# Kernel tuning notes

Hardware: AMD Instinct MI355X
Metric: run time of the kernel (lower is better)

Reference implementation:

```python
import jax, jax.numpy as jnp
import numpy as np

POS_THR = 0.01
EXPANSION = 0.3
HW_RATIO = 2.0


def setup_inputs() -> dict:
    key = jax.random.key(0)
    kp, kj, kv, kg, km = jax.random.split(key, 5)
    B, P, K, H, W = 16, 20, 17, 160, 160
    hm_pred = jax.random.uniform(kp, (B, K, H, W), dtype=jnp.float32)  # some above POS_THR
    gt = jax.random.uniform(kg, (B, K, H, W), dtype=jnp.float32)
    xy = jax.random.uniform(kj, (B, P, K, 2), dtype=jnp.float32) * jnp.array([W, H], jnp.float32)
    v = (jax.random.uniform(kv, (B, P, K, 1)) > 0.3).astype(jnp.float32)
    jointsXYV = jnp.concatenate([xy, v], axis=-1)
    masks = (jax.random.uniform(km, (B, H, W)) > 0.02).astype(jnp.float32)
    return {"hm_pred": hm_pred, "jointsXYV": jointsXYV, "masks": masks, "gt": gt}


def _gen_hm_mask(hm_pred, masks, jointsXYV):
    # hm_pred: [B,K,H,W]; masks: [B,H,W]; jointsXYV: [B,P,K,3]
    B, K, H, W = hm_pred.shape
    f32 = hm_pred.dtype
    vis = (jointsXYV[..., 2] > 0).any(axis=2)          # [B,P] person has any visible joint
    invisible = jointsXYV[..., 2] <= 0                 # [B,P,K]
    xy = jointsXYV[..., :2]                            # [B,P,K,2]
    inf = jnp.asarray(jnp.inf, f32)
    bb_TL = jnp.where(invisible[..., None], inf, xy).min(axis=2)    # [B,P,2]
    bb_BR = jnp.where(invisible[..., None], -inf, xy).max(axis=2)   # [B,P,2]
    bb_WH = jnp.maximum(bb_BR - bb_TL, 1.0)
    bb_CT = 0.5 * (bb_BR + bb_TL)
    bb_WH = jnp.maximum(bb_WH, bb_WH[..., ::-1] / HW_RATIO)
    half = (0.5 + EXPANSION) * bb_WH
    BR = jnp.round(bb_CT + half)
    TL = jnp.round(bb_CT - half)
    gy = jnp.arange(H, dtype=f32)[:, None]             # [H,1]
    gx = jnp.arange(W, dtype=f32)[None, :]             # [1,W]
    minx = TL[..., 0][:, :, None, None]
    miny = TL[..., 1][:, :, None, None]
    maxx = BR[..., 0][:, :, None, None]
    maxy = BR[..., 1][:, :, None, None]
    # True outside the person's expanded bbox  [B,P,H,W]
    outside = (gx < minx) | (gx > maxx) | (gy < miny) | (gy > maxy)
    # per-person per-keypoint mask: 1 keeps pixel; 0 suppresses inside-bbox pixels of
    # invisible keypoints. [B,P,K,H,W]
    paf = outside[:, :, None, :, :] | (~invisible)[:, :, :, None, None]
    # persons with no visible joint were filtered by nonzero() in torch -> neutral (all True)
    paf = paf | (~vis)[:, :, None, None, None]
    allp = paf.all(axis=1)                             # min-reduce over persons  [B,K,H,W]
    hm_masks = jnp.minimum(masks[:, None, :, :], allp.astype(f32))
    hm_masks = jnp.where(hm_pred >= POS_THR, jnp.asarray(1.0, f32), hm_masks)
    return hm_masks


def reference(hm_pred, jointsXYV, masks, gt):
    hm_masks = _gen_hm_mask(hm_pred, masks, jointsXYV)
    loss = (hm_pred - gt) ** 2 * hm_masks
    return loss.mean(axis=(1, 2, 3))  # per-image loss [B]
```

## Files before the change

### kernel.cpp

```cpp
#include <hip/hip_runtime.h>

#define BB 16
#define PP 20
#define KK 17
#define HH 160
#define WW 160
#define POS_THR 0.01f

struct Person {
    float minx, miny, maxx, maxy;
    unsigned int active;
    unsigned int invmask;
};


__global__ void prep_kernel(const float* __restrict__ joints, Person* __restrict__ persons,
                            float* __restrict__ acc) {
    int t = threadIdx.x;
    if (t < BB) acc[t] = 0.0f;
    if (t >= BB * PP) return;
    const float* j = joints + (size_t)t * KK * 3;
    float tlx = INFINITY, tly = INFINITY, brx = -INFINITY, bry = -INFINITY;
    unsigned int inv = 0;
    bool anyvis = false;
    for (int k = 0; k < KK; ++k) {
        float x = j[k * 3 + 0];
        float y = j[k * 3 + 1];
        float v = j[k * 3 + 2];
        if (v > 0.0f) {
            anyvis = true;
            tlx = fminf(tlx, x); tly = fminf(tly, y);
            brx = fmaxf(brx, x); bry = fmaxf(bry, y);
        } else {
            inv |= (1u << k);
        }
    }
    Person ps;
    if (!anyvis) {
        ps.active = 0; ps.invmask = 0;
        ps.minx = 0.0f; ps.miny = 0.0f; ps.maxx = -1.0f; ps.maxy = -1.0f;
    } else {
        float w0 = fmaxf(brx - tlx, 1.0f);
        float h0 = fmaxf(bry - tly, 1.0f);
        float cx = 0.5f * (brx + tlx);
        float cy = 0.5f * (bry + tly);
        float w1 = fmaxf(w0, h0 / 2.0f);
        float h1 = fmaxf(h0, w0 / 2.0f);
        float hx = (0.5f + 0.3f) * w1;
        float hy = (0.5f + 0.3f) * h1;
        ps.minx = rintf(cx - hx);
        ps.maxx = rintf(cx + hx);
        ps.miny = rintf(cy - hy);
        ps.maxy = rintf(cy + hy);
        ps.active = 1;
        ps.invmask = inv;
    }
    persons[t] = ps;
}

__global__ void __launch_bounds__(256) main_kernel(
        const float* __restrict__ hm, const float* __restrict__ gt,
        const float* __restrict__ masks, const Person* __restrict__ persons,
        float* __restrict__ acc) {
    const int pixPerB = HH * WW;
    const int blocksPerB = pixPerB / 256;
    int b = blockIdx.x / blocksPerB;
    int pix = (blockIdx.x % blocksPerB) * 256 + threadIdx.x;
    float gx = (float)(pix % WW);
    float gy = (float)(pix / WW);

    const Person* pp = persons + b * PP;
    unsigned int jmask = 0;
    #pragma unroll
    for (int p = 0; p < PP; ++p) {
        Person ps = pp[p];
        bool inside = (ps.active != 0u) &
                      (gx >= ps.minx) & (gx <= ps.maxx) &
                      (gy >= ps.miny) & (gy <= ps.maxy);
        if (inside) jmask |= ps.invmask;
    }

    float mv = masks[b * pixPerB + pix];
    float lsum = 0.0f;
    size_t base = (size_t)b * KK * pixPerB + pix;
    #pragma unroll
    for (int k = 0; k < KK; ++k) {
        float h = hm[base + (size_t)k * pixPerB];
        float g = gt[base + (size_t)k * pixPerB];
        float allp = ((jmask >> k) & 1u) ? 0.0f : 1.0f;
        float m = fminf(mv, allp);
        m = (h >= POS_THR) ? 1.0f : m;
        float d = h - g;
        lsum = fmaf(d * d, m, lsum);
    }

    #pragma unroll
    for (int off = 32; off > 0; off >>= 1) lsum += __shfl_down(lsum, off);
    __shared__ float wsum[4];
    int lane = threadIdx.x & 63;
    int wid = threadIdx.x >> 6;
    if (lane == 0) wsum[wid] = lsum;
    __syncthreads();
    if (threadIdx.x == 0) {
        float s = (wsum[0] + wsum[1]) + (wsum[2] + wsum[3]);
        atomicAdd(&acc[b], s);
    }
}

__global__ void finish_kernel(const float* __restrict__ acc, float* __restrict__ out) {
    int t = threadIdx.x;
    if (t < BB) out[t] = acc[t] / (float)(KK * HH * WW);
}

extern "C" void kernel_launch(void* const* d_in, const int* in_sizes, int n_in,
                              void* d_out, int out_size, void* d_ws, size_t ws_size,
                              hipStream_t stream) {
    const float* hm     = (const float*)d_in[0];
    const float* joints = (const float*)d_in[1];
    const float* masks  = (const float*)d_in[2];
    const float* gt     = (const float*)d_in[3];
    float* out = (float*)d_out;

    Person* persons = (Person*)d_ws;
    float* acc = (float*)((char*)d_ws + sizeof(Person) * BB * PP);

    prep_kernel<<<1, 384, 0, stream>>>(joints, persons, acc);
    main_kernel<<<BB * (HH * WW / 256), 256, 0, stream>>>(hm, gt, masks, persons, acc);
    finish_kernel<<<1, 64, 0, stream>>>(acc, out);
}
```

Measured before the change: 118.8 us.

## Fuse bbox prep into main kernel, vectorize to float4, drop atomics

Folds the per-person bounding box computation into each block's prologue via shared memory, removing the separate prep launch. Each thread now handles four consecutive pixels with float4 loads of heatmap, gt and mask. Per-block partials are written to a buffer and summed deterministically in the finish kernel instead of using atomicAdd. Every block redundantly recomputes person boxes for its image, and there are 4x fewer blocks, which lowers the number of waves in flight for a memory-bound kernel.

```diff
diff --git a/kernel.cpp b/kernel.cpp
--- a/kernel.cpp
+++ b/kernel.cpp
@@ -5,6 +5,12 @@
 #define KK 17
 #define HH 160
 #define WW 160
+#define PIX (HH * WW)
+#define TPB 256
+#define VPT 4
+#define PIXPERBLK (TPB * VPT)
+#define BLKPERB (PIX / PIXPERBLK)
+#define NBLK (BB * BLKPERB)
 #define POS_THR 0.01f
 
 struct Person {
@@ -14,84 +20,98 @@
 };
 
 
-__global__ void prep_kernel(const float* __restrict__ joints, Person* __restrict__ persons,
-                            float* __restrict__ acc) {
-    int t = threadIdx.x;
-    if (t < BB) acc[t] = 0.0f;
-    if (t >= BB * PP) return;
-    const float* j = joints + (size_t)t * KK * 3;
-    float tlx = INFINITY, tly = INFINITY, brx = -INFINITY, bry = -INFINITY;
-    unsigned int inv = 0;
-    bool anyvis = false;
-    for (int k = 0; k < KK; ++k) {
-        float x = j[k * 3 + 0];
-        float y = j[k * 3 + 1];
-        float v = j[k * 3 + 2];
-        if (v > 0.0f) {
-            anyvis = true;
-            tlx = fminf(tlx, x); tly = fminf(tly, y);
-            brx = fmaxf(brx, x); bry = fmaxf(bry, y);
+__global__ void __launch_bounds__(TPB) main_kernel(
+        const float* __restrict__ hm, const float* __restrict__ gt,
+        const float* __restrict__ masks, const float* __restrict__ joints,
+        float* __restrict__ partial) {
+    __shared__ Person sP[PP];
+    int b = blockIdx.x / BLKPERB;
+    int blk = blockIdx.x % BLKPERB;
+
+    if (threadIdx.x < PP) {
+        const float* j = joints + ((size_t)b * PP + threadIdx.x) * KK * 3;
+        float tlx = INFINITY, tly = INFINITY, brx = -INFINITY, bry = -INFINITY;
+        unsigned int inv = 0;
+        bool anyvis = false;
+        #pragma unroll
+        for (int k = 0; k < KK; ++k) {
+            float x = j[k * 3 + 0];
+            float y = j[k * 3 + 1];
+            float v = j[k * 3 + 2];
+            if (v > 0.0f) {
+                anyvis = true;
+                tlx = fminf(tlx, x); tly = fminf(tly, y);
+                brx = fmaxf(brx, x); bry = fmaxf(bry, y);
+            } else {
+                inv |= (1u << k);
+            }
+        }
+        Person ps;
+        if (!anyvis) {
+            ps.active = 0; ps.invmask = 0;
+            ps.minx = 0.0f; ps.miny = 0.0f; ps.maxx = -1.0f; ps.maxy = -1.0f;
         } else {
-            inv |= (1u << k);
+            float w0 = fmaxf(brx - tlx, 1.0f);
+            float h0 = fmaxf(bry - tly, 1.0f);
+            float cx = 0.5f * (brx + tlx);
+            float cy = 0.5f * (bry + tly);
+            float w1 = fmaxf(w0, h0 / 2.0f);
+            float h1 = fmaxf(h0, w0 / 2.0f);
+            float hx = (0.5f + 0.3f) * w1;
+            float hy = (0.5f + 0.3f) * h1;
+            ps.minx = rintf(cx - hx);
+            ps.maxx = rintf(cx + hx);
+            ps.miny = rintf(cy - hy);
+            ps.maxy = rintf(cy + hy);
+            ps.active = 1;
+            ps.invmask = inv;
+        }
+        sP[threadIdx.x] = ps;
+    }
+    __syncthreads();
+
+    int pix0 = blk * PIXPERBLK + threadIdx.x * VPT;
+    float gy = (float)(pix0 / WW);
+    int x0 = pix0 % WW;
+
+    unsigned int jm0 = 0, jm1 = 0, jm2 = 0, jm3 = 0;
+    #pragma unroll
+    for (int p = 0; p < PP; ++p) {
+        Person ps = sP[p];
+        bool iy = (ps.active != 0u) & (gy >= ps.miny) & (gy <= ps.maxy);
+        if (iy) {
+            float fx0 = (float)x0;
+            if ((fx0 >= ps.minx)        & (fx0 <= ps.maxx))        jm0 |= ps.invmask;
+            if ((fx0 + 1.0f >= ps.minx) & (fx0 + 1.0f <= ps.maxx)) jm1 |= ps.invmask;
+            if ((fx0 + 2.0f >= ps.minx) & (fx0 + 2.0f <= ps.maxx)) jm2 |= ps.invmask;
+            if ((fx0 + 3.0f >= ps.minx) & (fx0 + 3.0f <= ps.maxx)) jm3 |= ps.invmask;
         }
     }
-    Person ps;
-    if (!anyvis) {
-        ps.active = 0; ps.invmask = 0;
-        ps.minx = 0.0f; ps.miny = 0.0f; ps.maxx = -1.0f; ps.maxy = -1.0f;
-    } else {
-        float w0 = fmaxf(brx - tlx, 1.0f);
-        float h0 = fmaxf(bry - tly, 1.0f);
-        float cx = 0.5f * (brx + tlx);
-        float cy = 0.5f * (bry + tly);
-        float w1 = fmaxf(w0, h0 / 2.0f);
-        float h1 = fmaxf(h0, w0 / 2.0f);
-        float hx = (0.5f + 0.3f) * w1;
-        float hy = (0.5f + 0.3f) * h1;
-        ps.minx = rintf(cx - hx);
-        ps.maxx = rintf(cx + hx);
-        ps.miny = rintf(cy - hy);
-        ps.maxy = rintf(cy + hy);
-        ps.active = 1;
-        ps.invmask = inv;
-    }
-    persons[t] = ps;
-}
 
-__global__ void __launch_bounds__(256) main_kernel(
-        const float* __restrict__ hm, const float* __restrict__ gt,
-        const float* __restrict__ masks, const Person* __restrict__ persons,
-        float* __restrict__ acc) {
-    const int pixPerB = HH * WW;
-    const int blocksPerB = pixPerB / 256;
-    int b = blockIdx.x / blocksPerB;
-    int pix = (blockIdx.x % blocksPerB) * 256 + threadIdx.x;
-    float gx = (float)(pix % WW);
-    float gy = (float)(pix / WW);
+    const float4* m4 = (const float4*)(masks + (size_t)b * PIX);
+    float4 mv = m4[pix0 >> 2];
 
-    const Person* pp = persons + b * PP;
-    unsigned int jmask = 0;
-    #pragma unroll
-    for (int p = 0; p < PP; ++p) {
-        Person ps = pp[p];
-        bool inside = (ps.active != 0u) &
-                      (gx >= ps.minx) & (gx <= ps.maxx) &
-                      (gy >= ps.miny) & (gy <= ps.maxy);
-        if (inside) jmask |= ps.invmask;
-    }
-
-    float mv = masks[b * pixPerB + pix];
     float lsum = 0.0f;
-    size_t base = (size_t)b * KK * pixPerB + pix;
+    const size_t planeBase = (size_t)b * KK * PIX;
     #pragma unroll
     for (int k = 0; k < KK; ++k) {
-        float h = hm[base + (size_t)k * pixPerB];
-        float g = gt[base + (size_t)k * pixPerB];
-        float allp = ((jmask >> k) & 1u) ? 0.0f : 1.0f;
-        float m = fminf(mv, allp);
-        m = (h >= POS_THR) ? 1.0f : m;
-        float d = h - g;
-        lsum = fmaf(d * d, m, lsum);
+        const float4* h4 = (const float4*)(hm + planeBase + (size_t)k * PIX);
+        const float4* g4 = (const float4*)(gt + planeBase + (size_t)k * PIX);
+        float4 h = h4[pix0 >> 2];
+        float4 g = g4[pix0 >> 2];
+        float a0 = ((jm0 >> k) & 1u) ? 0.0f : 1.0f;
+        float a1 = ((jm1 >> k) & 1u) ? 0.0f : 1.0f;
+        float a2 = ((jm2 >> k) & 1u) ? 0.0f : 1.0f;
+        float a3 = ((jm3 >> k) & 1u) ? 0.0f : 1.0f;
+        float m0 = (h.x >= POS_THR) ? 1.0f : fminf(mv.x, a0);
+        float m1 = (h.y >= POS_THR) ? 1.0f : fminf(mv.y, a1);
+        float m2 = (h.z >= POS_THR) ? 1.0f : fminf(mv.z, a2);
+        float m3 = (h.w >= POS_THR) ? 1.0f : fminf(mv.w, a3);
+        float d0 = h.x - g.x, d1 = h.y - g.y, d2 = h.z - g.z, d3 = h.w - g.w;
+        lsum = fmaf(d0 * d0, m0, lsum);
+        lsum = fmaf(d1 * d1, m1, lsum);
+        lsum = fmaf(d2 * d2, m2, lsum);
+        lsum = fmaf(d3 * d3, m3, lsum);
     }
 
     #pragma unroll
@@ -102,14 +122,18 @@
     if (lane == 0) wsum[wid] = lsum;
     __syncthreads();
     if (threadIdx.x == 0) {
-        float s = (wsum[0] + wsum[1]) + (wsum[2] + wsum[3]);
-        atomicAdd(&acc[b], s);
+        partial[blockIdx.x] = (wsum[0] + wsum[1]) + (wsum[2] + wsum[3]);
     }
 }
 
-__global__ void finish_kernel(const float* __restrict__ acc, float* __restrict__ out) {
-    int t = threadIdx.x;
-    if (t < BB) out[t] = acc[t] / (float)(KK * HH * WW);
+__global__ void finish_kernel(const float* __restrict__ partial, float* __restrict__ out) {
+    int b = threadIdx.x;
+    if (b < BB) {
+        float s = 0.0f;
+        #pragma unroll
+        for (int i = 0; i < BLKPERB; ++i) s += partial[b * BLKPERB + i];
+        out[b] = s / (float)(KK * HH * WW);
+    }
 }
 
 extern "C" void kernel_launch(void* const* d_in, const int* in_sizes, int n_in,
@@ -120,11 +144,8 @@
     const float* masks  = (const float*)d_in[2];
     const float* gt     = (const float*)d_in[3];
     float* out = (float*)d_out;
+    float* partial = (float*)d_ws;
 
-    Person* persons = (Person*)d_ws;
-    float* acc = (float*)((char*)d_ws + sizeof(Person) * BB * PP);
-
-    prep_kernel<<<1, 384, 0, stream>>>(joints, persons, acc);
-    main_kernel<<<BB * (HH * WW / 256), 256, 0, stream>>>(hm, gt, masks, persons, acc);
-    finish_kernel<<<1, 64, 0, stream>>>(acc, out);
+    main_kernel<<<NBLK, TPB, 0, stream>>>(hm, gt, masks, joints, partial);
+    finish_kernel<<<1, 64, 0, stream>>>(partial, out);
 }
```

Result: faster. 99.94 us (-15.8%).
